# Kernel optimization log

Hardware: AMD Instinct MI355X
Metric: run time of the kernel (lower is better)

Reference implementation:

```python
import jax, jax.numpy as jnp
import numpy as np

N = 50000      # nodes
E = 800000     # edges
F_IN = 128     # input node features
HID = 96       # hidden_channels (heads=1 -> in_dim=HID)
L = 4          # num_layers
OUT = 1
EPS_SM = 1e-16 # PyG softmax eps


def layer_norm(x, g, b):
    mu = jnp.mean(x, axis=-1, keepdims=True)
    var = jnp.var(x, axis=-1, keepdims=True)
    return (x - mu) * jax.lax.rsqrt(var + 1e-5) * g + b


def gatv2_layer(h, src, dst, ea, Wl, bl, Wr, br, We, att, bias):
    # GATv2Conv, heads=1, concat=True, add_self_loops=False, edge_dim=1
    xl = h @ Wl + bl                      # [N, C] source transform (x_j)
    xr = h @ Wr + br                      # [N, C] target transform (x_i)
    e = xl[src] + xr[dst] + ea @ We       # [E, C]
    e = jax.nn.leaky_relu(e, 0.2)
    alpha = e @ att                       # [E]
    # softmax over incoming edges of each destination node
    m = jax.ops.segment_max(alpha, dst, num_segments=N)
    a = jnp.exp(alpha - m[dst])
    s = jax.ops.segment_sum(a, dst, num_segments=N)
    a = a / (s[dst] + EPS_SM)
    out = jax.ops.segment_sum(xl[src] * a[:, None], dst, num_segments=N)
    return out + bias


def setup_inputs() -> dict:
    key = jax.random.key(0)
    ks = jax.random.split(key, 24)
    sc_in = 1.0 / np.sqrt(F_IN)
    sc_h = 1.0 / np.sqrt(HID)
    inp = {
        "x": jax.random.normal(ks[0], (N, F_IN), jnp.float32),
        "edge_index": jax.random.randint(ks[1], (2, E), 0, N, jnp.int64),
        "edge_weight": jax.random.uniform(ks[2], (E,), jnp.float32),
        "enc_W": jax.random.normal(ks[3], (F_IN, HID), jnp.float32) * sc_in,
        "enc_b": jnp.zeros((HID,), jnp.float32),
        "Wl": jax.random.normal(ks[4], (L, HID, HID), jnp.float32) * sc_h,
        "bl": jnp.zeros((L, HID), jnp.float32),
        "Wr": jax.random.normal(ks[5], (L, HID, HID), jnp.float32) * sc_h,
        "br": jnp.zeros((L, HID), jnp.float32),
        "We": jax.random.normal(ks[6], (L, 1, HID), jnp.float32),
        "att": jax.random.normal(ks[7], (L, HID), jnp.float32) * sc_h,
        "bias": jnp.zeros((L, HID), jnp.float32),
        "ln_g": jnp.ones((L, HID), jnp.float32),
        "ln_b": jnp.zeros((L, HID), jnp.float32),
        "lnf_g": jnp.ones((HID,), jnp.float32),
        "lnf_b": jnp.zeros((HID,), jnp.float32),
        "fc_W": jax.random.normal(ks[8], (HID, OUT), jnp.float32) * sc_h,
        "fc_b": jnp.zeros((OUT,), jnp.float32),
    }
    return inp


def reference(x, edge_index, edge_weight, enc_W, enc_b, Wl, bl, Wr, br, We, att,
              bias, ln_g, ln_b, lnf_g, lnf_b, fc_W, fc_b):
    src, dst = edge_index[0], edge_index[1]
    ea = edge_weight[:, None]             # [E, 1] edge_attr
    h = x @ enc_W + enc_b                 # node encoder
    for i in range(L):                    # DeepGCNLayer block='res+'
        hn = jax.nn.relu(layer_norm(h, ln_g[i], ln_b[i]))
        h = h + gatv2_layer(hn, src, dst, ea, Wl[i], bl[i], Wr[i], br[i],
                            We[i], att[i], bias[i])
    h = jax.nn.relu(layer_norm(h, lnf_g, lnf_b))
    return h @ fc_W + fc_b
```

## Files before the change

### kernel.cpp

```cpp
#include <hip/hip_runtime.h>
#include <math.h>

#define NN 50000
#define EE 800000
#define FIN 128
#define HID 96
#define NL 4
#define CHUNK 1024

typedef __attribute__((ext_vector_type(8))) short short8;
typedef __attribute__((ext_vector_type(4))) float floatx4;
typedef __attribute__((ext_vector_type(2))) _Float16 half2v;

#define WPREP_L (NL * 2 * 9216)
#define WPREP_TOT (WPREP_L + 12288)

struct u96 { unsigned x, y, z; };

__device__ __forceinline__ unsigned short f32_to_bf16_rne(float x) {
    unsigned u = __float_as_uint(x);
    unsigned r = (u + 0x7FFFu + ((u >> 16) & 1u)) >> 16;
    return (unsigned short)r;
}
__device__ __forceinline__ float bf16_to_f32(unsigned short h) {
    return __uint_as_float(((unsigned)h) << 16);
}

__global__ void k_hist(const int* __restrict__ dst, int* __restrict__ deg, int E) {
    int e = blockIdx.x * blockDim.x + threadIdx.x;
    if (e < E) atomicAdd(&deg[dst[e]], 1);
}

__global__ void k_scan1(const int* __restrict__ deg, int* __restrict__ partials, int n) {
    __shared__ int lds[256];
    int t = threadIdx.x;
    int base = blockIdx.x * CHUNK + t * 4;
    int s = 0;
    #pragma unroll
    for (int q = 0; q < 4; q++) { int idx = base + q; if (idx < n) s += deg[idx]; }
    lds[t] = s; __syncthreads();
    for (int o = 128; o > 0; o >>= 1) { if (t < o) lds[t] += lds[t + o]; __syncthreads(); }
    if (t == 0) partials[blockIdx.x] = lds[0];
}

__global__ void k_scan_mid(int* partials, int nb, int* rowptr, int n) {
    int lane = threadIdx.x;
    int orig = (lane < nb) ? partials[lane] : 0;
    int v = orig;
    #pragma unroll
    for (int off = 1; off < 64; off <<= 1) {
        int u = __shfl_up(v, off);
        if (lane >= off) v += u;
    }
    if (lane < nb) partials[lane] = v - orig;
    if (lane == 63) rowptr[n] = v;
}

__global__ void k_scan3(const int* __restrict__ deg, const int* __restrict__ partials,
                        int* __restrict__ rowptr, int* __restrict__ cursor, int n) {
    __shared__ int lds[256];
    int t = threadIdx.x;
    int base = blockIdx.x * CHUNK + t * 4;
    int v[4];
    #pragma unroll
    for (int q = 0; q < 4; q++) { int idx = base + q; v[q] = (idx < n) ? deg[idx] : 0; }
    int tsum = v[0] + v[1] + v[2] + v[3];
    lds[t] = tsum; __syncthreads();
    for (int o = 1; o < 256; o <<= 1) {
        int add = (t >= o) ? lds[t - o] : 0;
        __syncthreads();
        lds[t] += add;
        __syncthreads();
    }
    int excl = lds[t] - tsum;
    int run = partials[blockIdx.x] + excl;
    #pragma unroll
    for (int q = 0; q < 4; q++) {
        int idx = base + q;
        if (idx < n) { rowptr[idx] = run; cursor[idx] = run; run += v[q]; }
    }
}

__global__ void k_scatter(const int* __restrict__ src, const int* __restrict__ dst,
                          const float* __restrict__ ew, int* __restrict__ cursor,
                          unsigned* __restrict__ epack, int E) {
    int e = blockIdx.x * blockDim.x + threadIdx.x;
    if (e < E) {
        int p = atomicAdd(&cursor[dst[e]], 1);
        _Float16 hw = (_Float16)ew[e];
        unsigned short wb = *(unsigned short*)&hw;
        epack[p] = (unsigned)src[e] | ((unsigned)wb << 16);
    }
}

__global__ void k_wprep_all(const float* __restrict__ Wl, const float* __restrict__ Wr,
                            const float* __restrict__ encW,
                            unsigned short* __restrict__ wf_hi, unsigned short* __restrict__ wf_lo,
                            unsigned short* __restrict__ we_hi, unsigned short* __restrict__ we_lo) {
    int t = blockIdx.x * blockDim.x + threadIdx.x;
    if (t < WPREP_L) {
        int within = t % 9216, pair = t / 9216;
        int lr = pair & 1, layer = pair >> 1;
        int j = within & 7;
        int lane = (within >> 3) & 63;
        int cs = within >> 9;
        int s = cs % 3, ct = cs / 3;
        int col = ct * 16 + (lane & 15);
        int k = s * 32 + (lane >> 4) * 8 + j;
        const float* W = (lr ? Wr : Wl) + (size_t)layer * HID * HID;
        float v = W[k * HID + col];
        unsigned short hi = f32_to_bf16_rne(v);
        wf_hi[t] = hi;
        wf_lo[t] = f32_to_bf16_rne(v - bf16_to_f32(hi));
    } else if (t < WPREP_TOT) {
        int u = t - WPREP_L;
        int j = u & 7;
        int lane = (u >> 3) & 63;
        int cs = u >> 9;
        int s = cs & 3, ct = cs >> 2;
        int col = ct * 16 + (lane & 15);
        int k = s * 32 + (lane >> 4) * 8 + j;
        float v = encW[k * HID + col];
        unsigned short hi = f32_to_bf16_rne(v);
        we_hi[u] = hi;
        we_lo[u] = f32_to_bf16_rne(v - bf16_to_f32(hi));
    }
}

__global__ __launch_bounds__(256) void k_enc_mfma(const float* __restrict__ x,
        const unsigned short* __restrict__ we_hi, const unsigned short* __restrict__ we_lo,
        const float* __restrict__ b,
        const float* __restrict__ lng, const float* __restrict__ lnb,
        float* __restrict__ h,
        unsigned short* __restrict__ hn_hi, unsigned short* __restrict__ hn_lo, int n) {
    int t = threadIdx.x;
    int wave = t >> 6, lane = t & 63;
    int quad = lane >> 4, lid = lane & 15;
    int r0 = blockIdx.x * 64 + wave * 16;
    int arow = r0 + lid; if (arow >= n) arow = n - 1;
    short8 aH[4], aL[4];
    #pragma unroll
    for (int s = 0; s < 4; s++) {
        float4 p0 = *(const float4*)(x + (size_t)arow * FIN + s * 32 + quad * 8);
        float4 p1 = *(const float4*)(x + (size_t)arow * FIN + s * 32 + quad * 8 + 4);
        float f[8] = {p0.x, p0.y, p0.z, p0.w, p1.x, p1.y, p1.z, p1.w};
        #pragma unroll
        for (int j = 0; j < 8; j++) {
            unsigned short hi = f32_to_bf16_rne(f[j]);
            aH[s][j] = (short)hi;
            aL[s][j] = (short)f32_to_bf16_rne(f[j] - bf16_to_f32(hi));
        }
    }
    floatx4 o[6];
    #pragma unroll
    for (int ct = 0; ct < 6; ct++) {
        floatx4 acc = {0.f, 0.f, 0.f, 0.f};
        #pragma unroll
        for (int s = 0; s < 4; s++) {
            short8 bH = *(const short8*)(we_hi + ((ct * 4 + s) * 64 + lane) * 8);
            short8 bL = *(const short8*)(we_lo + ((ct * 4 + s) * 64 + lane) * 8);
            acc = __builtin_amdgcn_mfma_f32_16x16x32_bf16(aH[s], bH, acc, 0, 0, 0);
            acc = __builtin_amdgcn_mfma_f32_16x16x32_bf16(aH[s], bL, acc, 0, 0, 0);
            acc = __builtin_amdgcn_mfma_f32_16x16x32_bf16(aL[s], bH, acc, 0, 0, 0);
        }
        float bv = b[ct * 16 + lid];
        #pragma unroll
        for (int rg = 0; rg < 4; rg++) o[ct][rg] = acc[rg] + bv;
    }
    #pragma unroll
    for (int rg = 0; rg < 4; rg++) {
        float s1 = 0.f, s2 = 0.f;
        #pragma unroll
        for (int ct = 0; ct < 6; ct++) { s1 += o[ct][rg]; s2 += o[ct][rg] * o[ct][rg]; }
        #pragma unroll
        for (int off = 1; off < 16; off <<= 1) {
            s1 += __shfl_xor(s1, off);
            s2 += __shfl_xor(s2, off);
        }
        float mu = s1 * (1.f / 96.f);
        float var = s2 * (1.f / 96.f) - mu * mu;
        float rs = rsqrtf(var + 1e-5f);
        int orow = r0 + quad * 4 + rg;
        if (orow < n) {
            #pragma unroll
            for (int ct = 0; ct < 6; ct++) {
                int col = ct * 16 + lid;
                float v = o[ct][rg];
                h[(size_t)orow * HID + col] = v;
                float y = fmaxf((v - mu) * rs * lng[col] + lnb[col], 0.f);
                unsigned short hi = f32_to_bf16_rne(y);
                hn_hi[(size_t)orow * HID + col] = hi;
                hn_lo[(size_t)orow * HID + col] = f32_to_bf16_rne(y - bf16_to_f32(hi));
            }
        }
    }
}

__global__ __launch_bounds__(256) void k_gemm2_mfma(
        const unsigned short* __restrict__ hn_hi, const unsigned short* __restrict__ hn_lo,
        const unsigned short* __restrict__ wf_hi, const unsigned short* __restrict__ wf_lo,
        const float* __restrict__ bl, const float* __restrict__ br,
        unsigned short* __restrict__ xl_h, unsigned short* __restrict__ xr_h, int n) {
    __shared__ unsigned short lh[9216];
    __shared__ unsigned short ll[9216];
    int t = threadIdx.x;
    int wave = t >> 6, lane = t & 63;
    int quad = lane >> 4, lid = lane & 15;
    int r0 = blockIdx.x * 64 + wave * 16;
    int arow = r0 + lid; if (arow >= n) arow = n - 1;
    short8 aH[3], aL[3];
    #pragma unroll
    for (int s = 0; s < 3; s++) {
        aH[s] = *(const short8*)(hn_hi + (size_t)arow * HID + s * 32 + quad * 8);
        aL[s] = *(const short8*)(hn_lo + (size_t)arow * HID + s * 32 + quad * 8);
    }
    for (int lr = 0; lr < 2; lr++) {
        const unsigned short* sh = wf_hi + lr * 9216;
        const unsigned short* sl = wf_lo + lr * 9216;
        __syncthreads();
        for (int u = t; u < 1152; u += 256) {
            *(short8*)(lh + u * 8) = *(const short8*)(sh + u * 8);
            *(short8*)(ll + u * 8) = *(const short8*)(sl + u * 8);
        }
        __syncthreads();
        const float* bias = lr ? br : bl;
        unsigned short* out = lr ? xr_h : xl_h;
        #pragma unroll
        for (int ct = 0; ct < 6; ct++) {
            floatx4 acc = {0.f, 0.f, 0.f, 0.f};
            #pragma unroll
            for (int s = 0; s < 3; s++) {
                short8 bH = *(const short8*)(lh + ((ct * 3 + s) * 64 + lane) * 8);
                short8 bL = *(const short8*)(ll + ((ct * 3 + s) * 64 + lane) * 8);
                acc = __builtin_amdgcn_mfma_f32_16x16x32_bf16(aH[s], bH, acc, 0, 0, 0);
                acc = __builtin_amdgcn_mfma_f32_16x16x32_bf16(aH[s], bL, acc, 0, 0, 0);
                acc = __builtin_amdgcn_mfma_f32_16x16x32_bf16(aL[s], bH, acc, 0, 0, 0);
            }
            int col = ct * 16 + lid;
            float bv = bias[col];
            #pragma unroll
            for (int rg = 0; rg < 4; rg++) {
                int orow = r0 + quad * 4 + rg;
                if (orow < n) {
                    _Float16 hv = (_Float16)(acc[rg] + bv);
                    out[(size_t)orow * HID + col] = *(unsigned short*)&hv;
                }
            }
        }
    }
}

__global__ __launch_bounds__(256) void k_gat_fused(
        const unsigned short* __restrict__ xl_h, const unsigned short* __restrict__ xr_h,
        const unsigned* __restrict__ ep, const int* __restrict__ rowptr,
        const float* __restrict__ We, const float* __restrict__ att, const float* __restrict__ bias,
        float* __restrict__ h,
        unsigned short* __restrict__ hn_hi, unsigned short* __restrict__ hn_lo,
        float* __restrict__ out_final,
        const float* __restrict__ g, const float* __restrict__ bt,
        const float* __restrict__ fcW, const float* __restrict__ fcb,
        int mode, int n) {
    int lane = threadIdx.x & 63;
    int node = blockIdx.x * 4 + (threadIdx.x >> 6);
    if (node >= n) return;
    int grp = lane >> 4, sub = lane & 15;
    int d0 = sub * 6;
    unsigned gOffB = (unsigned)(sub * 12);

    const float LOG2E = 1.4426950408889634f;
    union U6 { u96 u; half2v h2[3]; _Float16 hf[6]; };
    half2v we_h[3], at_h[3], xr_hv[3];
    {
        U6 xrw;
        xrw.u = *(const u96*)((const char*)xr_h + ((unsigned)node * 192u + gOffB));
        float2 a0 = *(const float2*)(We + d0);
        float2 a1 = *(const float2*)(We + d0 + 2);
        float2 a2 = *(const float2*)(We + d0 + 4);
        float2 c0 = *(const float2*)(att + d0);
        float2 c1 = *(const float2*)(att + d0 + 2);
        float2 c2 = *(const float2*)(att + d0 + 4);
        we_h[0] = half2v{(_Float16)a0.x, (_Float16)a0.y};
        we_h[1] = half2v{(_Float16)a1.x, (_Float16)a1.y};
        we_h[2] = half2v{(_Float16)a2.x, (_Float16)a2.y};
        at_h[0] = half2v{(_Float16)(c0.x*LOG2E), (_Float16)(c0.y*LOG2E)};
        at_h[1] = half2v{(_Float16)(c1.x*LOG2E), (_Float16)(c1.y*LOG2E)};
        at_h[2] = half2v{(_Float16)(c2.x*LOG2E), (_Float16)(c2.y*LOG2E)};
        #pragma unroll
        for (int j = 0; j < 3; j++) xr_hv[j] = xrw.h2[j];
    }
    const half2v c02 = half2v{(_Float16)0.2f, (_Float16)0.2f};

    int beg = rowptr[node], end = rowptr[node + 1];
    float ssum = 0.f;
    float acc[6];
    #pragma unroll
    for (int j = 0; j < 6; j++) acc[j] = 0.f;

    auto lq = [&](int p, u96& vraw, _Float16& wh, bool& val) {
        int pe = p + grp;
        val = pe < end;
        int pc = val ? pe : end - 1;
        unsigned e = ep[pc];
        unsigned short wb = (unsigned short)(e >> 16);
        wh = *(_Float16*)&wb;
        vraw = *(const u96*)((const char*)xl_h + ((e & 0xFFFFu) * 192u + gOffB));
    };
    auto proc = [&](const u96& vraw, _Float16 wh, bool val) {
        U6 cv; cv.u = vraw;
        half2v w2 = half2v{wh, wh};
        float q = 0.f;
        #pragma unroll
        for (int j = 0; j < 3; j++) {
            half2v t = cv.h2[j] + xr_hv[j];
            t = w2 * we_h[j] + t;
            half2v t2 = t * c02;
            t = __builtin_elementwise_max(t, t2);
#if __has_builtin(__builtin_amdgcn_fdot2)
            q = __builtin_amdgcn_fdot2(t, at_h[j], q, false);
#else
            q = fmaf((float)t[0], (float)at_h[j][0], q);
            q = fmaf((float)t[1], (float)at_h[j][1], q);
#endif
        }
        q += __shfl_xor(q, 1); q += __shfl_xor(q, 2);
        q += __shfl_xor(q, 4); q += __shfl_xor(q, 8);
        float e = val ? exp2f(q) : 0.f;
        ssum += e;
        #pragma unroll
        for (int j = 0; j < 6; j++) acc[j] = fmaf((float)cv.hf[j], e, acc[j]);
    };

    if (beg < end) {
        u96 vA, vB; _Float16 wA, wB; bool okA, okB;
        lq(beg,     vA, wA, okA);
        lq(beg + 4, vB, wB, okB);
        for (int p = beg; p < end; p += 8) {
            proc(vA, wA, okA);
            lq(p + 8, vA, wA, okA);
            proc(vB, wB, okB);
            lq(p + 12, vB, wB, okB);
        }
    }

    ssum += __shfl_xor(ssum, 16); ssum += __shfl_xor(ssum, 32);
    #pragma unroll
    for (int j = 0; j < 6; j++) {
        acc[j] += __shfl_xor(acc[j], 16);
        acc[j] += __shfl_xor(acc[j], 32);
    }
    float inv = 1.f / (ssum + 1e-16f);

    float nh[6];
    float s1 = 0.f, s2 = 0.f;
    {
        float2 h0 = *(const float2*)(h + (size_t)node * HID + d0);
        float2 h1 = *(const float2*)(h + (size_t)node * HID + d0 + 2);
        float2 h2 = *(const float2*)(h + (size_t)node * HID + d0 + 4);
        float2 b0 = *(const float2*)(bias + d0);
        float2 b1 = *(const float2*)(bias + d0 + 2);
        float2 b2 = *(const float2*)(bias + d0 + 4);
        float hv[6] = {h0.x, h0.y, h1.x, h1.y, h2.x, h2.y};
        float bv[6] = {b0.x, b0.y, b1.x, b1.y, b2.x, b2.y};
        #pragma unroll
        for (int j = 0; j < 6; j++) {
            nh[j] = hv[j] + acc[j] * inv + bv[j];
            s1 += nh[j];
            s2 += nh[j] * nh[j];
        }
    }
    #pragma unroll
    for (int off = 1; off < 16; off <<= 1) {
        s1 += __shfl_xor(s1, off);
        s2 += __shfl_xor(s2, off);
    }
    float mu = s1 * (1.f / 96.f);
    float var = s2 * (1.f / 96.f) - mu * mu;
    float rs = rsqrtf(var + 1e-5f);

    if (mode == 0) {
        if (grp == 0) {
            float2 g0 = *(const float2*)(g + d0);
            float2 g1 = *(const float2*)(g + d0 + 2);
            float2 g2 = *(const float2*)(g + d0 + 4);
            float2 t0 = *(const float2*)(bt + d0);
            float2 t1 = *(const float2*)(bt + d0 + 2);
            float2 t2 = *(const float2*)(bt + d0 + 4);
            float gv[6] = {g0.x, g0.y, g1.x, g1.y, g2.x, g2.y};
            float tv[6] = {t0.x, t0.y, t1.x, t1.y, t2.x, t2.y};
            *(float2*)(h + (size_t)node * HID + d0)     = make_float2(nh[0], nh[1]);
            *(float2*)(h + (size_t)node * HID + d0 + 2) = make_float2(nh[2], nh[3]);
            *(float2*)(h + (size_t)node * HID + d0 + 4) = make_float2(nh[4], nh[5]);
            unsigned hi[3], lo[3];
            #pragma unroll
            for (int j = 0; j < 3; j++) {
                float ox = fmaxf((nh[2*j]   - mu) * rs * gv[2*j]   + tv[2*j],   0.f);
                float oy = fmaxf((nh[2*j+1] - mu) * rs * gv[2*j+1] + tv[2*j+1], 0.f);
                unsigned short hx = f32_to_bf16_rne(ox), hy = f32_to_bf16_rne(oy);
                unsigned short lx = f32_to_bf16_rne(ox - bf16_to_f32(hx));
                unsigned short ly = f32_to_bf16_rne(oy - bf16_to_f32(hy));
                hi[j] = (unsigned)hx | ((unsigned)hy << 16);
                lo[j] = (unsigned)lx | ((unsigned)ly << 16);
            }
            u96 wh = {hi[0], hi[1], hi[2]};
            u96 wl = {lo[0], lo[1], lo[2]};
            *(u96*)((char*)hn_hi + 2 * ((size_t)node * HID + d0)) = wh;
            *(u96*)((char*)hn_lo + 2 * ((size_t)node * HID + d0)) = wl;
        }
    } else {
        float pacc = 0.f;
        {
            float2 g0 = *(const float2*)(g + d0);
            float2 g1 = *(const float2*)(g + d0 + 2);
            float2 g2 = *(const float2*)(g + d0 + 4);
            float2 t0 = *(const float2*)(bt + d0);
            float2 t1 = *(const float2*)(bt + d0 + 2);
            float2 t2 = *(const float2*)(bt + d0 + 4);
            float2 w0 = *(const float2*)(fcW + d0);
            float2 w1 = *(const float2*)(fcW + d0 + 2);
            float2 w2 = *(const float2*)(fcW + d0 + 4);
            float gv[6] = {g0.x, g0.y, g1.x, g1.y, g2.x, g2.y};
            float tv[6] = {t0.x, t0.y, t1.x, t1.y, t2.x, t2.y};
            float wv[6] = {w0.x, w0.y, w1.x, w1.y, w2.x, w2.y};
            #pragma unroll
            for (int j = 0; j < 6; j++) {
                float y = fmaxf((nh[j] - mu) * rs * gv[j] + tv[j], 0.f);
                pacc = fmaf(y, wv[j], pacc);
            }
        }
        #pragma unroll
        for (int off = 1; off < 16; off <<= 1) pacc += __shfl_xor(pacc, off);
        if (lane == 0) out_final[node] = pacc + fcb[0];
    }
}

extern "C" void kernel_launch(void* const* d_in, const int* in_sizes, int n_in,
                              void* d_out, int out_size, void* d_ws, size_t ws_size,
                              hipStream_t stream) {
    const float* x    = (const float*)d_in[0];
    const int*   ei   = (const int*)  d_in[1];
    const float* ew   = (const float*)d_in[2];
    const float* encW = (const float*)d_in[3];
    const float* encB = (const float*)d_in[4];
    const float* Wl   = (const float*)d_in[5];
    const float* bl   = (const float*)d_in[6];
    const float* Wr   = (const float*)d_in[7];
    const float* br   = (const float*)d_in[8];
    const float* We   = (const float*)d_in[9];
    const float* att  = (const float*)d_in[10];
    const float* bias = (const float*)d_in[11];
    const float* lng  = (const float*)d_in[12];
    const float* lnb  = (const float*)d_in[13];
    const float* lnfg = (const float*)d_in[14];
    const float* lnfb = (const float*)d_in[15];
    const float* fcW  = (const float*)d_in[16];
    const float* fcb  = (const float*)d_in[17];
    float* out = (float*)d_out;

    const int* src = ei;
    const int* dst = ei + EE;

    char* ws = (char*)d_ws;
    size_t off = 0;
    auto alloc = [&](size_t bytes) -> void* {
        void* p = ws + off;
        off += (bytes + 255) & ~(size_t)255;
        return p;
    };
    float* h      = (float*)alloc((size_t)NN * HID * 4);
    unsigned short* xl_h  = (unsigned short*)alloc((size_t)NN * HID * 2 + 256);
    unsigned short* xr_h  = (unsigned short*)alloc((size_t)NN * HID * 2 + 256);
    unsigned short* hn_hi = (unsigned short*)alloc((size_t)NN * HID * 2);
    unsigned short* hn_lo = (unsigned short*)alloc((size_t)NN * HID * 2);
    unsigned short* wf_hi = (unsigned short*)alloc((size_t)WPREP_L * 2);
    unsigned short* wf_lo = (unsigned short*)alloc((size_t)WPREP_L * 2);
    unsigned short* we_hi = (unsigned short*)alloc(12288 * 2);
    unsigned short* we_lo = (unsigned short*)alloc(12288 * 2);
    int*   deg    = (int*)  alloc((size_t)NN * 4);
    int*   rowptr = (int*)  alloc((size_t)(NN + 1) * 4);
    int*   cursor = (int*)  alloc((size_t)NN * 4);
    unsigned* epack = (unsigned*)alloc((size_t)EE * 4);
    int*   parts  = (int*)  alloc(256 * 4);

    const int NB = (NN + CHUNK - 1) / CHUNK;
    const int EB = (EE + 255) / 256;
    const int MB = (NN + 63) / 64;
    const int WB = (NN + 3) / 4;

    hipMemsetAsync(deg, 0, (size_t)NN * 4, stream);
    k_hist<<<EB, 256, 0, stream>>>(dst, deg, EE);
    k_scan1<<<NB, 256, 0, stream>>>(deg, parts, NN);
    k_scan_mid<<<1, 64, 0, stream>>>(parts, NB, rowptr, NN);
    k_scan3<<<NB, 256, 0, stream>>>(deg, parts, rowptr, cursor, NN);
    k_scatter<<<EB, 256, 0, stream>>>(src, dst, ew, cursor, epack, EE);

    k_wprep_all<<<(WPREP_TOT + 255) / 256, 256, 0, stream>>>(Wl, Wr, encW, wf_hi, wf_lo, we_hi, we_lo);

    k_enc_mfma<<<MB, 256, 0, stream>>>(x, we_hi, we_lo, encB, lng, lnb, h, hn_hi, hn_lo, NN);

    for (int l = 0; l < NL; l++) {
        k_gemm2_mfma<<<MB, 256, 0, stream>>>(hn_hi, hn_lo,
            wf_hi + (size_t)l * 2 * 9216, wf_lo + (size_t)l * 2 * 9216,
            bl + l * HID, br + l * HID, xl_h, xr_h, NN);
        if (l < NL - 1) {
            k_gat_fused<<<WB, 256, 0, stream>>>(xl_h, xr_h, epack, rowptr,
                We + l * HID, att + l * HID, bias + l * HID,
                h, hn_hi, hn_lo, (float*)nullptr,
                lng + (l + 1) * HID, lnb + (l + 1) * HID,
                (const float*)nullptr, (const float*)nullptr, 0, NN);
        } else {
            k_gat_fused<<<WB, 256, 0, stream>>>(xl_h, xr_h, epack, rowptr,
                We + l * HID, att + l * HID, bias + l * HID,
                h, (unsigned short*)nullptr, (unsigned short*)nullptr, out,
                lnfg, lnfb, fcW, fcb, 1, NN);
        }
    }
}
```

Measured before the change: 475.6 us.

## Replace global-atomic CSR scatter with two-pass bucketed binning scatter

Replaces the per-edge global atomic scatter into CSR order with two passes. The first pass bins edges by destination node range (512 nodes per bucket) using shared-memory atomics and writes them to per-bucket staging buffers. The second pass places each bucket's edges using LDS cursors seeded from rowptr. This is meant to cut global atomic contention and random writes, at the cost of an extra staging buffer and a fixed bucket capacity that could overflow on skewed degree distributions.

```diff
diff --git a/kernel.cpp b/kernel.cpp
--- a/kernel.cpp
+++ b/kernel.cpp
@@ -14,6 +14,10 @@
 
 #define WPREP_L (NL * 2 * 9216)
 #define WPREP_TOT (WPREP_L + 12288)
+
+#define PH1E 4096
+#define NBUCK 98
+#define BCAP 9216
 
 struct u96 { unsigned x, y, z; };
 
@@ -81,15 +85,66 @@
     }
 }
 
-__global__ void k_scatter(const int* __restrict__ src, const int* __restrict__ dst,
-                          const float* __restrict__ ew, int* __restrict__ cursor,
-                          unsigned* __restrict__ epack, int E) {
-    int e = blockIdx.x * blockDim.x + threadIdx.x;
-    if (e < E) {
-        int p = atomicAdd(&cursor[dst[e]], 1);
-        _Float16 hw = (_Float16)ew[e];
-        unsigned short wb = *(unsigned short*)&hw;
-        epack[p] = (unsigned)src[e] | ((unsigned)wb << 16);
+__global__ __launch_bounds__(256) void k_binscatter(const int* __restrict__ src,
+        const int* __restrict__ dst, const float* __restrict__ ew,
+        int* __restrict__ gcur, uint2* __restrict__ ibuf, int E) {
+    __shared__ uint2 st[PH1E];
+    __shared__ int cnt[NBUCK], off[NBUCK], cur[NBUCK], gbase[NBUCK];
+    int t = threadIdx.x;
+    int e0 = blockIdx.x * PH1E;
+    for (int i = t; i < NBUCK; i += 256) { cnt[i] = 0; cur[i] = 0; }
+    __syncthreads();
+    #pragma unroll
+    for (int k = 0; k < PH1E / 256; k++) {
+        int e = e0 + k * 256 + t;
+        if (e < E) atomicAdd(&cnt[dst[e] >> 9], 1);
+    }
+    __syncthreads();
+    if (t == 0) {
+        int run = 0;
+        for (int b = 0; b < NBUCK; b++) { off[b] = run; run += cnt[b]; }
+    }
+    __syncthreads();
+    #pragma unroll
+    for (int k = 0; k < PH1E / 256; k++) {
+        int e = e0 + k * 256 + t;
+        if (e < E) {
+            int d = dst[e];
+            int b = d >> 9;
+            int p = off[b] + atomicAdd(&cur[b], 1);
+            _Float16 hw = (_Float16)ew[e];
+            unsigned short wb = *(unsigned short*)&hw;
+            st[p] = make_uint2((unsigned)d, (unsigned)src[e] | ((unsigned)wb << 16));
+        }
+    }
+    __syncthreads();
+    if (t < NBUCK) gbase[t] = atomicAdd(&gcur[t], cur[t]);
+    __syncthreads();
+    int total = min(PH1E, E - e0);
+    for (int i = t; i < total; i += 256) {
+        uint2 v = st[i];
+        int b = v.x >> 9;
+        ibuf[(size_t)b * BCAP + gbase[b] + (i - off[b])] = v;
+    }
+}
+
+__global__ __launch_bounds__(256) void k_binplace(const uint2* __restrict__ ibuf,
+        const int* __restrict__ gcur, const int* __restrict__ rowptr,
+        unsigned* __restrict__ epack, int n) {
+    __shared__ int cur[512];
+    int t = threadIdx.x;
+    int b = blockIdx.x;
+    int n0 = b << 9;
+    for (int i = t; i < 512; i += 256) {
+        int node = n0 + i;
+        cur[i] = (node < n) ? rowptr[node] : 0;
+    }
+    __syncthreads();
+    int nb = gcur[b];
+    for (int i = t; i < nb; i += 256) {
+        uint2 v = ibuf[(size_t)b * BCAP + i];
+        int p = atomicAdd(&cur[(int)v.x - n0], 1);
+        epack[p] = v.y;
     }
 }
 
@@ -479,19 +534,24 @@
     int*   rowptr = (int*)  alloc((size_t)(NN + 1) * 4);
     int*   cursor = (int*)  alloc((size_t)NN * 4);
     unsigned* epack = (unsigned*)alloc((size_t)EE * 4);
+    uint2* ibuf   = (uint2*)alloc((size_t)NBUCK * BCAP * 8);
+    int*   gcur   = (int*)  alloc(NBUCK * 4);
     int*   parts  = (int*)  alloc(256 * 4);
 
     const int NB = (NN + CHUNK - 1) / CHUNK;
     const int EB = (EE + 255) / 256;
+    const int PB = (EE + PH1E - 1) / PH1E;
     const int MB = (NN + 63) / 64;
     const int WB = (NN + 3) / 4;
 
     hipMemsetAsync(deg, 0, (size_t)NN * 4, stream);
+    hipMemsetAsync(gcur, 0, NBUCK * 4, stream);
     k_hist<<<EB, 256, 0, stream>>>(dst, deg, EE);
+    k_binscatter<<<PB, 256, 0, stream>>>(src, dst, ew, gcur, ibuf, EE);
     k_scan1<<<NB, 256, 0, stream>>>(deg, parts, NN);
     k_scan_mid<<<1, 64, 0, stream>>>(parts, NB, rowptr, NN);
     k_scan3<<<NB, 256, 0, stream>>>(deg, parts, rowptr, cursor, NN);
-    k_scatter<<<EB, 256, 0, stream>>>(src, dst, ew, cursor, epack, EE);
+    k_binplace<<<NBUCK, 256, 0, stream>>>(ibuf, gcur, rowptr, epack, NN);
 
     k_wprep_all<<<(WPREP_TOT + 255) / 256, 256, 0, stream>>>(Wl, Wr, encW, wf_hi, wf_lo, we_hi, we_lo);
 
```

After: 451.3 us. 1.05x faster.
